# Kernel optimization log

Hardware: AMD Instinct MI355X
Metric: run time of the kernel (lower is better)

The kernel has to match this reference:

```python
import jax, jax.numpy as jnp
import numpy as np

D_MODEL, D_K, D_V = 1024, 64, 128
NUM_HEAD = D_MODEL // D_V  # 8


def setup_inputs() -> dict:
    key = jax.random.key(0)
    ks = jax.random.split(key, 6)
    B, SQ, SKV = 4, 2048, 2048
    return {
        "encoder_output": jax.random.normal(ks[0], (B, SKV, D_MODEL), jnp.float32),
        "pre_output": jax.random.normal(ks[1], (B, SQ, D_MODEL), jnp.float32),
        "Wq": jax.random.normal(ks[2], (D_MODEL, D_K * NUM_HEAD), jnp.float32) * 0.02,
        "Wk": jax.random.normal(ks[3], (D_MODEL, D_K * NUM_HEAD), jnp.float32) * 0.02,
        "Wv": jax.random.normal(ks[4], (D_MODEL, D_MODEL), jnp.float32) * 0.02,
        "Wo": jax.random.normal(ks[5], (D_MODEL, D_MODEL), jnp.float32) * 0.02,
    }


def reference(encoder_output, pre_output, Wq, Wk, Wv, Wo):
    B, SQ, _ = pre_output.shape
    SKV = encoder_output.shape[1]
    # projections (Linear, bias=False)
    q = pre_output @ Wq          # [B, SQ, H*d_k]
    k = encoder_output @ Wk      # [B, SKV, H*d_k]
    v = encoder_output @ Wv      # [B, SKV, H*d_v] (= d_model)
    # per-head contiguous slices == reshape into head dim
    q = q.reshape(B, SQ, NUM_HEAD, D_K)
    k = k.reshape(B, SKV, NUM_HEAD, D_K)
    v = v.reshape(B, SKV, NUM_HEAD, D_V)
    scale = 1.0 / np.sqrt(D_K).astype(np.float32)
    scores = jnp.einsum("bqhd,bkhd->bhqk", q, k) * scale  # [B,H,SQ,SKV]
    attn = jax.nn.softmax(scores, axis=-1)
    out = jnp.einsum("bhqk,bkhd->bqhd", attn, v)           # [B,SQ,H,d_v]
    out = out.reshape(B, SQ, NUM_HEAD * D_V)               # concat heads
    return out @ Wo
```

## Files before the change

### kernel.cpp

```cpp
#include <hip/hip_runtime.h>
#include <math.h>

#define D_MODEL 1024
#define DK 64
#define DV 128
#define NH 8
#define BB 4
#define SQL 2048
#define SKV 2048

typedef __bf16 bf16x8 __attribute__((ext_vector_type(8)));
typedef float f32x4 __attribute__((ext_vector_type(4)));

#if __has_builtin(__builtin_amdgcn_exp2f)
#define EXP2(x) __builtin_amdgcn_exp2f(x)
#else
#define EXP2(x) exp2f(x)
#endif

#define MFMA16(a, b, c) __builtin_amdgcn_mfma_f32_16x16x32_bf16(a, b, c, 0, 0, 0)

__device__ __forceinline__ ushort f2bf(float f) {
  unsigned u = __float_as_uint(f);
  u += 0x7FFFu + ((u >> 16) & 1u);
  return (ushort)(u >> 16);
}
__device__ __forceinline__ unsigned pk2bf(float lo, float hi) {
  unsigned ul = __float_as_uint(lo);
  unsigned uh = __float_as_uint(hi);
  ul += 0x7FFFu + ((ul >> 16) & 1u);
  uh += 0x7FFFu + ((uh >> 16) & 1u);
  return __builtin_amdgcn_perm(uh, ul, 0x07060302u);
}

#define GLDS16(g, l)                                                       \
  __builtin_amdgcn_global_load_lds(                                        \
      (const __attribute__((address_space(1))) unsigned int*)(g),          \
      (__attribute__((address_space(3))) unsigned int*)(l), 16, 0, 0)

__global__ __launch_bounds__(256) void cvt2_kernel(
    const float* __restrict__ s0, const float* __restrict__ s1,
    ushort* __restrict__ d0, ushort* __restrict__ d1, int n4) {
  const float* src = blockIdx.z ? s1 : s0;
  ushort* dst = blockIdx.z ? d1 : d0;
  int i = blockIdx.x * 256 + threadIdx.x;
  if (i >= n4) return;
  float4 v = ((const float4*)src)[i];
  ushort4 o;
  o.x = f2bf(v.x); o.y = f2bf(v.y); o.z = f2bf(v.z); o.w = f2bf(v.w);
  ((ushort4*)dst)[i] = o;
}

__global__ __launch_bounds__(256) void cvt_t4_kernel(
    const float* __restrict__ W0, const float* __restrict__ W1,
    const float* __restrict__ W2, const float* __restrict__ W3,
    ushort* __restrict__ T0, ushort* __restrict__ T1, ushort* __restrict__ T2,
    ushort* __restrict__ T3) {
  __shared__ ushort T[32][34];
  const int z = blockIdx.z;
  const int C = (z < 2) ? 512 : 1024;
  const int c0 = blockIdx.y * 32;
  if (c0 >= C) return;
  const float* W = (z == 0) ? W0 : (z == 1) ? W1 : (z == 2) ? W2 : W3;
  ushort* Wt = (z == 0) ? T0 : (z == 1) ? T1 : (z == 2) ? T2 : T3;
  const int R = 1024;
  const int r0 = blockIdx.x * 32;
  const int tx = threadIdx.x, ty = threadIdx.y;
#pragma unroll
  for (int i = 0; i < 4; ++i) {
    const int rr = ty + i * 8;
    T[rr][tx] = f2bf(W[(size_t)(r0 + rr) * C + c0 + tx]);
  }
  __syncthreads();
#pragma unroll
  for (int i = 0; i < 4; ++i) {
    const int rr = ty + i * 8;
    Wt[(size_t)(c0 + rr) * R + r0 + tx] = T[tx][rr];
  }
}

__device__ __forceinline__ void gemm_core_acc(ushort* sh, const ushort* At,
                                              const ushort* Bt, int K,
                                              f32x4 (&acc)[4][4]) {
  const int t = threadIdx.x;
  const int w = t >> 6, lane = t & 63;
  const int wm = (w >> 1) * 64, wn = (w & 1) * 64;
  const int lr = lane & 15, quad = lane >> 4;

  const int r0 = t >> 2;
  const int lb = (t & 3) ^ ((r0 >> 1) & 3);
  const ushort* gA0 = At + (size_t)r0 * K + lb * 8;
  const ushort* gA1 = At + (size_t)(r0 + 64) * K + lb * 8;
  const ushort* gB0 = Bt + (size_t)r0 * K + lb * 8;
  const ushort* gB1 = Bt + (size_t)(r0 + 64) * K + lb * 8;

  const int sw = (quad ^ ((lr >> 1) & 3)) * 8;

#pragma unroll
  for (int i = 0; i < 4; ++i)
#pragma unroll
    for (int j = 0; j < 4; ++j) acc[i][j] = (f32x4){0.f, 0.f, 0.f, 0.f};

  auto stage = [&](int k0, int buf) {
    ushort* d = sh + buf * 8192 + t * 8;
    GLDS16(gA0 + k0, d);
    GLDS16(gA1 + k0, d + 2048);
    GLDS16(gB0 + k0, d + 4096);
    GLDS16(gB1 + k0, d + 6144);
  };

  stage(0, 0);
  __syncthreads();

  for (int k0 = 0; k0 < K; k0 += 32) {
    const int cur = (k0 >> 5) & 1;
    const bool more = (k0 + 32 < K);
    if (more) stage(k0 + 32, cur ^ 1);
    const ushort(*A)[32] = (const ushort(*)[32])(sh + cur * 8192);
    const ushort(*B)[32] = (const ushort(*)[32])(sh + cur * 8192 + 4096);
    bf16x8 fa[4], fb[4];
#pragma unroll
    for (int i = 0; i < 4; ++i) fa[i] = *(const bf16x8*)&A[wm + i * 16 + lr][sw];
#pragma unroll
    for (int j = 0; j < 4; ++j) fb[j] = *(const bf16x8*)&B[wn + j * 16 + lr][sw];
#pragma unroll
    for (int i = 0; i < 4; ++i)
#pragma unroll
      for (int j = 0; j < 4; ++j) acc[i][j] = MFMA16(fa[i], fb[j], acc[i][j]);
    if (more) __syncthreads();
  }
}

__global__ __launch_bounds__(256) void gemm_qkv_kernel(
    const ushort* __restrict__ preb, const ushort* __restrict__ encb,
    const ushort* __restrict__ WqkvT, ushort* __restrict__ qb,
    ushort* __restrict__ kb, ushort* __restrict__ vt, float qsc) {
  __shared__ __attribute__((aligned(16))) ushort shm[17408];

  const int n0 = blockIdx.x * 128, m0 = blockIdx.y * 128;
  const int t = threadIdx.x;
  const int w = t >> 6, lane = t & 63;
  const int wm = (w >> 1) * 64, wn = (w & 1) * 64;
  const int lr = lane & 15, quad = lane >> 4;

  const ushort* A = (n0 < 512) ? preb : encb;
  f32x4 acc[4][4];
  gemm_core_acc(shm, A + (size_t)m0 * D_MODEL, WqkvT + (size_t)n0 * D_MODEL,
                D_MODEL, acc);

  if (n0 < 1024) {
    ushort* C = (n0 < 512) ? qb : kb;
    const int ncol = (n0 < 512) ? n0 : n0 - 512;
    const float osc = (n0 < 512) ? qsc : 1.f;
#pragma unroll
    for (int i = 0; i < 4; ++i)
#pragma unroll
      for (int j = 0; j < 4; ++j)
#pragma unroll
        for (int r = 0; r < 4; ++r) {
          const int row = m0 + wm + i * 16 + quad * 4 + r;
          const int col = ncol + wn + j * 16 + lr;
          C[(size_t)row * 512 + col] = f2bf(acc[i][j][r] * osc);
        }
  } else {
    const int h = (n0 - 1024) >> 7;
    const int b = m0 >> 11;
    const int skv0 = m0 & 2047;
    __syncthreads();
    ushort(*Ep)[68] = (ushort(*)[68])(shm + w * 4352);
#pragma unroll
    for (int i = 0; i < 4; ++i)
#pragma unroll
      for (int j = 0; j < 4; ++j) {
        uint2 dd;
        dd.x = pk2bf(acc[i][j][0], acc[i][j][1]);
        dd.y = pk2bf(acc[i][j][2], acc[i][j][3]);
        *(uint2*)&Ep[j * 16 + lr][i * 16 + quad * 4] = dd;
      }
    ushort* vbase =
        vt + ((size_t)(b * NH + h) * DV + wn) * SKV + skv0 + wm;
#pragma unroll
    for (int rep = 0; rep < 8; ++rep) {
      const int dvl = (lane >> 3) + rep * 8;
      const int skvc = (lane & 7) * 8;
      *(uint4*)&vbase[(size_t)dvl * SKV + skvc] = *(const uint4*)&Ep[dvl][skvc];
    }
  }
}

__global__ __launch_bounds__(256) void gemm_o_kernel(
    const ushort* __restrict__ ao, const ushort* __restrict__ WoT,
    float* __restrict__ out) {
  __shared__ __attribute__((aligned(16))) ushort sh[16384];
  const int n0 = blockIdx.x * 128, m0 = blockIdx.y * 128;
  const int t = threadIdx.x;
  const int w = t >> 6, lane = t & 63;
  const int wm = (w >> 1) * 64, wn = (w & 1) * 64;
  const int lr = lane & 15, quad = lane >> 4;
  f32x4 acc[4][4];
  gemm_core_acc(sh, ao + (size_t)m0 * D_MODEL, WoT + (size_t)n0 * D_MODEL,
                D_MODEL, acc);
#pragma unroll
  for (int i = 0; i < 4; ++i)
#pragma unroll
    for (int j = 0; j < 4; ++j)
#pragma unroll
      for (int r = 0; r < 4; ++r) {
        const int row = m0 + wm + i * 16 + quad * 4 + r;
        const int col = n0 + wn + j * 16 + lr;
        out[(size_t)row * D_MODEL + col] = acc[i][j][r];
      }
}

__global__ __launch_bounds__(256) void attn_mfma_kernel(
    const ushort* __restrict__ Q, const ushort* __restrict__ Kb,
    const ushort* __restrict__ Vt, ushort* __restrict__ Oo) {
  __shared__ ushort Ks[2][64][64];
  __shared__ ushort Vs[2][128][64];
  __shared__ ushort Ps[4][32][36];

  const int t = threadIdx.x;
  const int n = blockIdx.x + 16 * blockIdx.y + 128 * blockIdx.z;
  const int l = (n & 7) * 64 + (n >> 3);
  const int qt = l & 15, h = (l >> 4) & 7, b = l >> 7;

  const int w = t >> 6, lane = t & 63;
  const int lr = lane & 15, quad = lane >> 4;
  const int q0 = qt * 128 + w * 32;
  const int swk = lr & 7;

  union { bf16x8 v; ushort u[8]; } one8;
#pragma unroll
  for (int i = 0; i < 8; ++i) one8.u[i] = 0x3F80;

  bf16x8 aq[2][2];
#pragma unroll
  for (int mt = 0; mt < 2; ++mt)
#pragma unroll
    for (int kh = 0; kh < 2; ++kh)
      aq[mt][kh] = *(const bf16x8*)&Q[(size_t)(b * SQL + q0 + mt * 16 + lr) *
                                          (NH * DK) +
                                      h * DK + kh * 32 + quad * 8];

  f32x4 accO[2][9];
#pragma unroll
  for (int mt = 0; mt < 2; ++mt)
#pragma unroll
    for (int dn = 0; dn < 9; ++dn) accO[mt][dn] = (f32x4){0.f, 0.f, 0.f, 0.f};

  const ushort* kbase = Kb + (size_t)b * SKV * (NH * DK) + h * DK;
  const ushort* vbase = Vt + (size_t)(b * NH + h) * DV * SKV;

  const int srow = t >> 3;
  const int sb7 = (t & 7) ^ (srow & 7);
  const ushort* gK = kbase + (size_t)srow * (NH * DK) + sb7 * 8;
  const ushort* gV = vbase + (size_t)srow * SKV + sb7 * 8;
  ushort* dK = (ushort*)Ks + t * 8;
  ushort* dV = (ushort*)Vs + t * 8;

  auto stage = [&](int kv0, int buf) {
    const ushort* gk = gK + (size_t)kv0 * (NH * DK);
    ushort* dk = dK + buf * 4096;
    GLDS16(gk, dk);
    GLDS16(gk + (size_t)32 * (NH * DK), dk + 2048);
    const ushort* gv = gV + kv0;
    ushort* dv = dV + buf * 8192;
    GLDS16(gv, dv);
    GLDS16(gv + (size_t)32 * SKV, dv + 2048);
    GLDS16(gv + (size_t)64 * SKV, dv + 4096);
    GLDS16(gv + (size_t)96 * SKV, dv + 6144);
  };

  auto chunk = [&](const ushort(*Kc)[64], const ushort(*Vc)[64], int c) {
#pragma unroll
    for (int tt = 0; tt < 2; ++tt) {
      const int nt = c * 2 + tt;
      const bf16x8 fk0 = *(const bf16x8*)&Kc[nt * 16 + lr][(quad ^ swk) * 8];
      const bf16x8 fk1 =
          *(const bf16x8*)&Kc[nt * 16 + lr][((4 + quad) ^ swk) * 8];
#pragma unroll
      for (int mt = 0; mt < 2; ++mt) {
        f32x4 s = (f32x4){0.f, 0.f, 0.f, 0.f};
        s = MFMA16(fk0, aq[mt][0], s);
        s = MFMA16(fk1, aq[mt][1], s);
        const unsigned u0 = __float_as_uint(EXP2(s[0]));
        const unsigned u1 = __float_as_uint(EXP2(s[1]));
        const unsigned u2 = __float_as_uint(EXP2(s[2]));
        const unsigned u3 = __float_as_uint(EXP2(s[3]));
        uint2 dd;
        dd.x = __builtin_amdgcn_perm(u1, u0, 0x07060302u);
        dd.y = __builtin_amdgcn_perm(u3, u2, 0x07060302u);
        *(uint2*)&Ps[w][mt * 16 + lr][tt * 16 + quad * 4] = dd;
      }
    }
    bf16x8 ap[2];
#pragma unroll
    for (int mt = 0; mt < 2; ++mt) {
      union { bf16x8 v; uint2 u[2]; } fr;
      fr.u[0] = *(const uint2*)&Ps[w][mt * 16 + lr][quad * 8];
      fr.u[1] = *(const uint2*)&Ps[w][mt * 16 + lr][quad * 8 + 4];
      ap[mt] = fr.v;
    }
    __builtin_amdgcn_s_setprio(1);
#pragma unroll
    for (int dn = 0; dn < 8; ++dn) {
      const bf16x8 fv =
          *(const bf16x8*)&Vc[dn * 16 + lr][((c * 4 + quad) ^ swk) * 8];
      accO[0][dn] = MFMA16(ap[0], fv, accO[0][dn]);
      accO[1][dn] = MFMA16(ap[1], fv, accO[1][dn]);
    }
    accO[0][8] = MFMA16(ap[0], one8.v, accO[0][8]);
    accO[1][8] = MFMA16(ap[1], one8.v, accO[1][8]);
    __builtin_amdgcn_s_setprio(0);
  };

  stage(0, 0);
  for (int ti = 0; ti < 31; ++ti) {
    stage((ti + 1) * 64, (ti + 1) & 1);
    asm volatile("s_waitcnt vmcnt(6)" ::: "memory");
    __builtin_amdgcn_s_barrier();
    __builtin_amdgcn_sched_barrier(0);
    const ushort(*Kc)[64] = Ks[ti & 1];
    const ushort(*Vc)[64] = Vs[ti & 1];
    chunk(Kc, Vc, 0);
    chunk(Kc, Vc, 1);
    __builtin_amdgcn_sched_barrier(0);
    __builtin_amdgcn_s_barrier();
  }
  asm volatile("s_waitcnt vmcnt(0)" ::: "memory");
  __builtin_amdgcn_s_barrier();
  __builtin_amdgcn_sched_barrier(0);
  chunk(Ks[1], Vs[1], 0);
  chunk(Ks[1], Vs[1], 1);

#pragma unroll
  for (int mt = 0; mt < 2; ++mt) {
    float inv[4];
#pragma unroll
    for (int r = 0; r < 4; ++r) inv[r] = 1.f / accO[mt][8][r];
#pragma unroll
    for (int dn = 0; dn < 8; ++dn)
#pragma unroll
      for (int r = 0; r < 4; ++r) {
        const size_t row = (size_t)b * SQL + q0 + mt * 16 + quad * 4 + r;
        Oo[row * D_MODEL + h * DV + dn * 16 + lr] =
            f2bf(accO[mt][dn][r] * inv[r]);
      }
  }
}

extern "C" void kernel_launch(void* const* d_in, const int* in_sizes, int n_in,
                              void* d_out, int out_size, void* d_ws,
                              size_t ws_size, hipStream_t stream) {
  const float* enc = (const float*)d_in[0];
  const float* pre = (const float*)d_in[1];
  const float* Wq = (const float*)d_in[2];
  const float* Wk = (const float*)d_in[3];
  const float* Wv = (const float*)d_in[4];
  const float* Wo = (const float*)d_in[5];
  float* out = (float*)d_out;

  const int M = BB * SQL;

  ushort* encb = (ushort*)d_ws;
  ushort* preb = encb + (size_t)M * D_MODEL;
  ushort* WqT = preb + (size_t)M * D_MODEL;
  ushort* WkT = WqT + (size_t)(NH * DK) * D_MODEL;
  ushort* WvT = WkT + (size_t)(NH * DK) * D_MODEL;
  ushort* WoT = WvT + (size_t)D_MODEL * D_MODEL;
  ushort* qb = WoT + (size_t)D_MODEL * D_MODEL;
  ushort* kb = qb + (size_t)M * (NH * DK);
  ushort* vt = kb + (size_t)M * (NH * DK);
  ushort* ao = encb;

  const int n4 = M * D_MODEL / 4;
  dim3 blk(256);
  dim3 tblk(32, 8);

  cvt2_kernel<<<dim3(n4 / 256, 1, 2), blk, 0, stream>>>(enc, pre, encb, preb,
                                                        n4);
  cvt_t4_kernel<<<dim3(32, 32, 4), tblk, 0, stream>>>(Wq, Wk, Wv, Wo, WqT, WkT,
                                                      WvT, WoT);

  gemm_qkv_kernel<<<dim3(16, 64), blk, 0, stream>>>(
      preb, encb, WqT, qb, kb, vt, 0.18033688011112042f);

  attn_mfma_kernel<<<dim3(SQL / 128, NH, BB), blk, 0, stream>>>(qb, kb, vt, ao);

  gemm_o_kernel<<<dim3(8, 64), blk, 0, stream>>>(ao, WoT, out);
}
```

Baseline: 260.1 us.

## Use explicit vmcnt waits and raw barriers in GEMM loop; remap blocks per XCD

```diff
diff --git a/kernel.cpp b/kernel.cpp
--- a/kernel.cpp
+++ b/kernel.cpp
@@ -109,15 +109,20 @@
     GLDS16(gB1 + k0, d + 6144);
   };
 
+  const int NT = K >> 5;
   stage(0, 0);
-  __syncthreads();
-
-  for (int k0 = 0; k0 < K; k0 += 32) {
-    const int cur = (k0 >> 5) & 1;
-    const bool more = (k0 + 32 < K);
-    if (more) stage(k0 + 32, cur ^ 1);
-    const ushort(*A)[32] = (const ushort(*)[32])(sh + cur * 8192);
-    const ushort(*B)[32] = (const ushort(*)[32])(sh + cur * 8192 + 4096);
+  for (int ti = 0; ti < NT; ++ti) {
+    const bool more = (ti + 1 < NT);
+    if (more) {
+      stage((ti + 1) * 32, (ti + 1) & 1);
+      asm volatile("s_waitcnt vmcnt(4)" ::: "memory");
+    } else {
+      asm volatile("s_waitcnt vmcnt(0)" ::: "memory");
+    }
+    __builtin_amdgcn_s_barrier();
+    __builtin_amdgcn_sched_barrier(0);
+    const ushort(*A)[32] = (const ushort(*)[32])(sh + (ti & 1) * 8192);
+    const ushort(*B)[32] = (const ushort(*)[32])(sh + (ti & 1) * 8192 + 4096);
     bf16x8 fa[4], fb[4];
 #pragma unroll
     for (int i = 0; i < 4; ++i) fa[i] = *(const bf16x8*)&A[wm + i * 16 + lr][sw];
@@ -127,7 +132,8 @@
     for (int i = 0; i < 4; ++i)
 #pragma unroll
       for (int j = 0; j < 4; ++j) acc[i][j] = MFMA16(fa[i], fb[j], acc[i][j]);
-    if (more) __syncthreads();
+    __builtin_amdgcn_sched_barrier(0);
+    if (more) __builtin_amdgcn_s_barrier();
   }
 }
 
@@ -137,7 +143,10 @@
     ushort* __restrict__ kb, ushort* __restrict__ vt, float qsc) {
   __shared__ __attribute__((aligned(16))) ushort shm[17408];
 
-  const int n0 = blockIdx.x * 128, m0 = blockIdx.y * 128;
+  const int nlin = blockIdx.x + 16 * blockIdx.y;
+  const int l = (nlin & 7) * 128 + (nlin >> 3);
+  const int n0 = (l & 15) * 128, m0 = (l >> 4) * 128;
+
   const int t = threadIdx.x;
   const int w = t >> 6, lane = t & 63;
   const int wm = (w >> 1) * 64, wn = (w & 1) * 64;
@@ -192,7 +201,9 @@
     const ushort* __restrict__ ao, const ushort* __restrict__ WoT,
     float* __restrict__ out) {
   __shared__ __attribute__((aligned(16))) ushort sh[16384];
-  const int n0 = blockIdx.x * 128, m0 = blockIdx.y * 128;
+  const int nlin = blockIdx.x + 8 * blockIdx.y;
+  const int l = (nlin & 7) * 64 + (nlin >> 3);
+  const int n0 = (l & 7) * 128, m0 = (l >> 3) * 128;
   const int t = threadIdx.x;
   const int w = t >> 6, lane = t & 63;
   const int wm = (w >> 1) * 64, wn = (w & 1) * 64;
```

Result: no change. 257.6 us (median of 2 runs) (-1.0%).
